# Kernel optimization log

Hardware: AMD Instinct MI355X
Metric: run time of the kernel (lower is better)

## Reference

```python
import jax, jax.numpy as jnp
import numpy as np

D_MODEL = 768
N_HEADS = 12
D_K = 768
D_V = 768
SEQ = 2048
BATCH = 2


def setup_inputs() -> dict:
    key = jax.random.key(0)
    ks = jax.random.split(key, 9)
    s = 0.02
    return {
        "x": jax.random.normal(ks[0], (SEQ, BATCH, D_MODEL), dtype=jnp.float32),
        "Wq": jax.random.normal(ks[1], (D_MODEL, D_K), dtype=jnp.float32) * s,
        "bq": jnp.zeros((D_K,), dtype=jnp.float32),
        "Wk": jax.random.normal(ks[2], (D_MODEL, D_K), dtype=jnp.float32) * s,
        "bk": jnp.zeros((D_K,), dtype=jnp.float32),
        "Wv": jax.random.normal(ks[3], (D_MODEL, D_V), dtype=jnp.float32) * s,
        "bv": jnp.zeros((D_V,), dtype=jnp.float32),
        "Wo": jax.random.normal(ks[4], (D_V, D_MODEL), dtype=jnp.float32) * s,
        "bo": jnp.zeros((D_MODEL,), dtype=jnp.float32),
    }


def reference(x, Wq, bq, Wk, bk, Wv, bv, Wo, bo):
    # x: (S, B, D)
    S, B, D = x.shape
    H = N_HEADS
    hk = D_K // H
    hv = D_V // H
    q = (x @ Wq + bq).reshape(S, B, H, hk)
    k = (x @ Wk + bk).reshape(S, B, H, hk)
    v = (x @ Wv + bv).reshape(S, B, H, hv)
    scale = 1.0 / np.sqrt(hk).astype(np.float32)
    # scores: (B, H, S_q, S_k)
    att = jnp.einsum("sbhd,tbhd->bhst", q, k) * scale
    causal = jnp.triu(jnp.ones((S, S), dtype=bool), k=1)  # True above diagonal
    att = jnp.where(causal, jnp.float32(-jnp.inf), att)
    att = jax.nn.softmax(att, axis=-1)
    y = jnp.einsum("bhst,tbhd->sbhd", att, v).reshape(S, B, D_V)
    return y @ Wo + bo  # (S, B, D)
```

## Files before the change

### kernel.cpp

```cpp
#include <hip/hip_runtime.h>

typedef __attribute__((ext_vector_type(8))) short short8;
typedef __attribute__((ext_vector_type(4))) float f32x4;

#define NHEADS 12
#define SEQLEN 2048
#define HEADD  64
#define DMODEL 768

__device__ __forceinline__ short cvtbf(float f) {
  unsigned u = __builtin_bit_cast(unsigned, f);
  u += 0x7fffu + ((u >> 16) & 1u);
  return (short)(u >> 16);
}

__device__ __forceinline__ void gload16(const void* g, void* l) {
  __builtin_amdgcn_global_load_lds((const __attribute__((address_space(1))) void*)g,
                                   (__attribute__((address_space(3))) void*)l, 16, 0, 0);
}

__device__ __forceinline__ void ds_write_hi16(short* p, float v) {
  asm volatile("ds_write_b16_d16_hi %0, %1"
               : : "v"((__attribute__((address_space(3))) short*)p), "v"(v) : "memory");
}

__global__ void cvt_x_kernel(const float* __restrict__ x, short* __restrict__ o) {
  int i = blockIdx.x * 256 + threadIdx.x;
  const float* p = x + (size_t)i * 8;
  short8 v;
#pragma unroll
  for (int j = 0; j < 8; ++j) v[j] = cvtbf(p[j]);
  *(short8*)(o + (size_t)i * 8) = v;
}

__global__ void transpose_w_kernel(const float* __restrict__ w0, const float* __restrict__ w1,
                                   const float* __restrict__ w2, const float* __restrict__ w3,
                                   short* __restrict__ wt, short* __restrict__ wot) {
  __shared__ float t[32][33];
  const float* W = blockIdx.z == 0 ? w0 : blockIdx.z == 1 ? w1 : blockIdx.z == 2 ? w2 : w3;
  short* O = blockIdx.z < 3 ? wt + (size_t)blockIdx.z * (768 * 768) : wot;
  int tx = threadIdx.x, ty = threadIdx.y;
  int n0 = blockIdx.x * 32, k0 = blockIdx.y * 32;
#pragma unroll
  for (int j = 0; j < 4; ++j)
    t[ty + j * 8][tx] = W[(k0 + ty + j * 8) * 768 + n0 + tx];
  __syncthreads();
#pragma unroll
  for (int j = 0; j < 4; ++j)
    O[(n0 + ty + j * 8) * 768 + k0 + tx] = cvtbf(t[tx][ty + j * 8]);
}

template <int BN>
__device__ __forceinline__ void gemm_core64(const short* __restrict__ A,
                                            const short* __restrict__ Bt,
                                            short* sA, short* sB,
                                            int bm, int bn, f32x4 acc[2][BN / 32]) {
  constexpr int NT = BN / 32;
  const int tid = threadIdx.x;
  const int w = tid >> 6, lane = tid & 63;
  const int quad = lane >> 4, l16 = lane & 15;
  const int wm = (w & 1) * 32, wn = (w >> 1) * (BN / 2);

  int gA[2], lA[2], gB[NT], lB[NT];
#pragma unroll
  for (int j = 0; j < 2; ++j) {
    int slot = j * 256 + w * 64 + lane;
    int r = slot >> 3, c = (slot & 7) ^ (r & 7);
    gA[j] = (bm * 64 + r) * 768 + c * 8;
    lA[j] = (j * 256 + w * 64) * 8;
  }
#pragma unroll
  for (int j = 0; j < NT; ++j) {
    int slot = j * 256 + w * 64 + lane;
    int r = slot >> 3, c = (slot & 7) ^ (r & 7);
    gB[j] = (bn * BN + r) * 768 + c * 8;
    lB[j] = (j * 256 + w * 64) * 8;
  }

  for (int kt = 0; kt < 12; ++kt) {
    __syncthreads();
#pragma unroll
    for (int j = 0; j < 2; ++j) gload16(A + gA[j] + kt * 64, sA + lA[j]);
#pragma unroll
    for (int j = 0; j < NT; ++j) gload16(Bt + gB[j] + kt * 64, sB + lB[j]);
    __syncthreads();
#pragma unroll
    for (int ks = 0; ks < 2; ++ks) {
      short8 a[2], b[NT];
      int cp = (ks * 4 + quad) ^ (l16 & 7);
#pragma unroll
      for (int mt = 0; mt < 2; ++mt)
        a[mt] = *(const short8*)(sA + (wm + mt * 16 + l16) * 64 + cp * 8);
#pragma unroll
      for (int nt = 0; nt < NT; ++nt)
        b[nt] = *(const short8*)(sB + (wn + nt * 16 + l16) * 64 + cp * 8);
#pragma unroll
      for (int mt = 0; mt < 2; ++mt)
#pragma unroll
        for (int nt = 0; nt < NT; ++nt)
          acc[mt][nt] = __builtin_amdgcn_mfma_f32_16x16x32_bf16(a[mt], b[nt], acc[mt][nt], 0, 0, 0);
    }
  }
}

__global__ __launch_bounds__(256, 4) void qkv_gemm(
    const short* __restrict__ A, const short* __restrict__ Bt,
    const float* __restrict__ bq, const float* __restrict__ bk, const float* __restrict__ bv,
    short* __restrict__ oq, short* __restrict__ ok, short* __restrict__ ov) {
  __shared__ short sA[64 * 64];
  __shared__ short sB[128 * 64];
  f32x4 acc[2][4];
  const f32x4 z4 = {0.f, 0.f, 0.f, 0.f};
#pragma unroll
  for (int mt = 0; mt < 2; ++mt)
#pragma unroll
    for (int nt = 0; nt < 4; ++nt) acc[mt][nt] = z4;

  const int bm = blockIdx.x, bn = blockIdx.y;
  gemm_core64<128>(A, Bt, sA, sB, bm, bn, acc);

  const int seg = bn / 6, bn_l = bn % 6;
  const float* bias = seg == 0 ? bq : seg == 1 ? bk : bv;
  short* outp = seg == 0 ? oq : seg == 1 ? ok : ov;

  const int tid = threadIdx.x;
  const int w = tid >> 6, lane = tid & 63;
  const int quad = lane >> 4, l16 = lane & 15;
  const int wm = (w & 1) * 32, wn = (w >> 1) * 64;

#pragma unroll
  for (int nt = 0; nt < 4; ++nt) {
    int n = bn_l * 128 + wn + nt * 16 + l16;
    float bval = bias[n];
    int h = n >> 6, d = n & 63;
#pragma unroll
    for (int mt = 0; mt < 2; ++mt) {
      int rowb = wm + mt * 16 + quad * 4;
#pragma unroll
      for (int r = 0; r < 4; ++r) {
        int m = bm * 64 + rowb + r;
        int s = m >> 1, b = m & 1;
        float v = acc[mt][nt][r] + bval;
        if (seg == 0) v *= 0.1803368801f;
        if (seg < 2)
          outp[((b * NHEADS + h) * SEQLEN + s) * HEADD + d] = cvtbf(v);
        else
          outp[((b * NHEADS + h) * HEADD + d) * SEQLEN + s] = cvtbf(v);
      }
    }
  }
}

#define AE(qi, ts, nt) ((qi) | ((ts) << 8) | ((nt) << 16))
__device__ const int ATTN_TAB[80] = {
  AE(31,0,8), AE(31,8,8), AE(31,16,8), AE(31,24,8),
  AE(30,0,8), AE(30,8,8), AE(30,16,8),
  AE(29,0,8), AE(29,8,8), AE(29,16,8),
  AE(28,0,8), AE(28,8,8), AE(28,16,8),
  AE(27,0,8), AE(27,8,8), AE(27,16,8),
  AE(26,0,8), AE(26,8,8), AE(26,16,8),
  AE(25,0,8), AE(25,8,8), AE(25,16,8),
  AE(24,0,8), AE(24,8,8), AE(24,16,8),
  AE(23,0,8), AE(23,8,8), AE(23,16,8),
  AE(22,0,8), AE(22,8,8),
  AE(21,0,8), AE(21,8,8),
  AE(20,0,8), AE(20,8,8),
  AE(19,0,8), AE(19,8,8),
  AE(18,0,8), AE(18,8,8),
  AE(17,0,8), AE(17,8,8),
  AE(16,0,8), AE(16,8,8),
  AE(15,0,8), AE(15,8,8),
  AE(14,0,8), AE(13,0,8), AE(12,0,8), AE(11,0,8),
  AE(10,0,8), AE(9,0,8),  AE(8,0,8),  AE(7,0,8),
  AE(30,24,7), AE(22,16,7), AE(14,8,7), AE(6,0,7),
  AE(29,24,6), AE(21,16,6), AE(13,8,6), AE(5,0,6),
  AE(28,24,5), AE(20,16,5), AE(12,8,5), AE(4,0,5),
  AE(27,24,4), AE(19,16,4), AE(11,8,4), AE(3,0,4),
  AE(26,24,3), AE(18,16,3), AE(10,8,3), AE(2,0,3),
  AE(25,24,2), AE(17,16,2), AE(9,8,2),  AE(1,0,2),
  AE(24,24,1), AE(16,16,1), AE(8,8,1),  AE(0,0,1),
};
__device__ const int PBASE[32] = {
  0,0,0,0,0,0,0,0,
  0,2,4,6,8,10,12,14,
  16,19,22,25,28,31,34,37,
  40,44,48,52,56,60,64,68};

__global__ __launch_bounds__(256, 4) void attn_kernel(
    const short* __restrict__ Q, const short* __restrict__ K,
    const short* __restrict__ Vt, short* __restrict__ Y,
    float* __restrict__ Of, float* __restrict__ lf) {
  __shared__ short sK[2][64 * 64];
  __shared__ short sV[2][64 * 64];
  __shared__ short sP[64 * 64];
  const int tid = threadIdx.x;
  const int w = tid >> 6, lane = tid & 63;
  const int quad = lane >> 4, l16 = lane & 15;
  const int e = ATTN_TAB[blockIdx.x / 24];
  const int bh = blockIdx.x % 24;
  const int qi = e & 255, ts = (e >> 8) & 255, ntl = e >> 16;
  const int q0 = qi << 6;
  const short* Qb = Q + (size_t)bh * (SEQLEN * HEADD);
  const short* Kb = K + (size_t)bh * (SEQLEN * HEADD);
  const short* Vb = Vt + (size_t)bh * (SEQLEN * HEADD);

  short8 aq[2];
#pragma unroll
  for (int ks = 0; ks < 2; ++ks)
    aq[ks] = *(const short8*)(Qb + (q0 + w * 16 + l16) * 64 + ks * 32 + quad * 8);

  const short8 bones = {0x3F80, 0x3F80, 0x3F80, 0x3F80, 0x3F80, 0x3F80, 0x3F80, 0x3F80};
  f32x4 acc_o[4], acc_l;
  const f32x4 z4 = {0.f, 0.f, 0.f, 0.f};
#pragma unroll
  for (int nt = 0; nt < 4; ++nt) acc_o[nt] = z4;
  acc_l = z4;

  int gK[2], gV[2], lbase[2];
#pragma unroll
  for (int j = 0; j < 2; ++j) {
    int slot = j * 256 + w * 64 + lane;
    int r = slot >> 3, c = (slot & 7) ^ (r & 7);
    gK[j] = r * 64 + c * 8;
    gV[j] = r * 2048 + c * 8;
    lbase[j] = (j * 256 + w * 64) * 8;
  }

  const int qrow = q0 + w * 16 + quad * 4;
  const int tend = ts + ntl;

#pragma unroll
  for (int j = 0; j < 2; ++j) {
    gload16(Kb + (ts << 6) * 64 + gK[j], &sK[0][lbase[j]]);
    gload16(Vb + (ts << 6) + gV[j], &sV[0][lbase[j]]);
  }

  int pb = 0;
  for (int it = ts; it < tend; ++it) {
    __syncthreads();
    if (it + 1 < tend) {
      const int t1 = (it + 1) << 6;
#pragma unroll
      for (int j = 0; j < 2; ++j) {
        gload16(Kb + t1 * 64 + gK[j], &sK[pb ^ 1][lbase[j]]);
        gload16(Vb + t1 + gV[j], &sV[pb ^ 1][lbase[j]]);
      }
    }
    const short* sk = sK[pb];
    const short* sv = sV[pb];

    f32x4 sc[4];
#pragma unroll
    for (int nt = 0; nt < 4; ++nt) sc[nt] = z4;
#pragma unroll
    for (int ks = 0; ks < 2; ++ks) {
      int cp = (ks * 4 + quad) ^ (l16 & 7);
#pragma unroll
      for (int nt = 0; nt < 4; ++nt) {
        short8 bk = *(const short8*)(sk + (nt * 16 + l16) * 64 + cp * 8);
        sc[nt] = __builtin_amdgcn_mfma_f32_16x16x32_bf16(aq[ks], bk, sc[nt], 0, 0, 0);
      }
    }

    if (it == qi) {
      const int t0 = it << 6;
#pragma unroll
      for (int nt = 0; nt < 4; ++nt)
#pragma unroll
        for (int r = 0; r < 4; ++r) {
          int t = t0 + nt * 16 + l16;
          if (t > qrow + r) sc[nt][r] = -1e30f;
        }
    }

#pragma unroll
    for (int nt = 0; nt < 4; ++nt)
#pragma unroll
      for (int r = 0; r < 4; ++r) {
        float p = __builtin_amdgcn_exp2f(sc[nt][r]);
        int rq = w * 16 + quad * 4 + r;
        int t = nt * 16 + l16;
        int c = t >> 3;
        ds_write_hi16(&sP[rq * 64 + ((c ^ (rq & 7)) * 8 + (t & 7))], p);
      }

#pragma unroll
    for (int kst = 0; kst < 2; ++kst) {
      int rq = w * 16 + l16;
      int cpa = (kst * 4 + quad) ^ (rq & 7);
      short8 ap = *(const short8*)(sP + rq * 64 + cpa * 8);
      acc_l = __builtin_amdgcn_mfma_f32_16x16x32_bf16(ap, bones, acc_l, 0, 0, 0);
#pragma unroll
      for (int nt = 0; nt < 4; ++nt) {
        int row = nt * 16 + l16;
        int cv = (kst * 4 + quad) ^ (row & 7);
        short8 bv = *(const short8*)(sv + row * 64 + cv * 8);
        acc_o[nt] = __builtin_amdgcn_mfma_f32_16x16x32_bf16(ap, bv, acc_o[nt], 0, 0, 0);
      }
    }
    pb ^= 1;
  }

  if (qi < 8) {
    const int b = bh / NHEADS, h = bh % NHEADS;
#pragma unroll
    for (int r = 0; r < 4; ++r) {
      float rl = __builtin_amdgcn_rcpf(acc_l[r]);
      int srow = q0 + w * 16 + quad * 4 + r;
#pragma unroll
      for (int nt = 0; nt < 4; ++nt)
        Y[(srow * 2 + b) * DMODEL + h * 64 + nt * 16 + l16] = cvtbf(acc_o[nt][r] * rl);
    }
  } else {
    const int slot = bh * 72 + PBASE[qi] + (ts >> 3);
    float* Ob = Of + (size_t)slot * 4096;
#pragma unroll
    for (int r = 0; r < 4; ++r) {
      int row = w * 16 + quad * 4 + r;
#pragma unroll
      for (int nt = 0; nt < 4; ++nt)
        Ob[row * 64 + nt * 16 + l16] = acc_o[nt][r];
      if (l16 == 0) lf[slot * 64 + row] = acc_l[r];
    }
  }
}

__global__ void attn_merge(const float* __restrict__ Of, const float* __restrict__ lf,
                           short* __restrict__ Y) {
  const int bh = blockIdx.x % 24, qi = 8 + blockIdx.x / 24;
  const int nch = (qi >> 3) + 1;
  const int base = bh * 72 + PBASE[qi];
  const float* O0 = Of + (size_t)base * 4096;
  const float* L0 = lf + base * 64;
  const int b = bh / NHEADS, h = bh % NHEADS;
  const int tid = threadIdx.x;
#pragma unroll
  for (int j = 0; j < 16; ++j) {
    int idx = j * 256 + tid;
    int row = idx >> 6, col = idx & 63;
    float o = 0.f, l = 0.f;
    for (int c = 0; c < nch; ++c) {
      o += O0[c * 4096 + idx];
      l += L0[c * 64 + row];
    }
    float v = o * __builtin_amdgcn_rcpf(l);
    int srow = qi * 64 + row;
    Y[(srow * 2 + b) * DMODEL + h * 64 + col] = cvtbf(v);
  }
}

__global__ __launch_bounds__(256, 4) void oproj_gemm(
    const short* __restrict__ A, const short* __restrict__ Bt,
    const float* __restrict__ bo, float* __restrict__ out) {
  __shared__ short sA[64 * 64];
  __shared__ short sB[64 * 64];
  f32x4 acc[2][2];
  const f32x4 z4 = {0.f, 0.f, 0.f, 0.f};
#pragma unroll
  for (int mt = 0; mt < 2; ++mt)
#pragma unroll
    for (int nt = 0; nt < 2; ++nt) acc[mt][nt] = z4;

  const int bm = blockIdx.x, bn = blockIdx.y;
  gemm_core64<64>(A, Bt, sA, sB, bm, bn, acc);

  const int tid = threadIdx.x;
  const int w = tid >> 6, lane = tid & 63;
  const int quad = lane >> 4, l16 = lane & 15;
  const int wm = (w & 1) * 32, wn = (w >> 1) * 32;

#pragma unroll
  for (int nt = 0; nt < 2; ++nt) {
    int n = bn * 64 + wn + nt * 16 + l16;
    float bval = bo[n];
#pragma unroll
    for (int mt = 0; mt < 2; ++mt) {
      int rowb = wm + mt * 16 + quad * 4;
#pragma unroll
      for (int r = 0; r < 4; ++r) {
        int m = bm * 64 + rowb + r;
        out[(size_t)m * 768 + n] = acc[mt][nt][r] + bval;
      }
    }
  }
}

extern "C" void kernel_launch(void* const* d_in, const int* in_sizes, int n_in,
                              void* d_out, int out_size, void* d_ws, size_t ws_size,
                              hipStream_t stream) {
  const float* x  = (const float*)d_in[0];
  const float* Wq = (const float*)d_in[1];
  const float* bq = (const float*)d_in[2];
  const float* Wk = (const float*)d_in[3];
  const float* bk = (const float*)d_in[4];
  const float* Wv = (const float*)d_in[5];
  const float* bv = (const float*)d_in[6];
  const float* Wo = (const float*)d_in[7];
  const float* bo = (const float*)d_in[8];
  float* out = (float*)d_out;

  short* ws  = (short*)d_ws;
  short* xb  = ws;
  short* wt  = ws + 3145728;
  short* wot = ws + 4915200;
  short* qw  = ws + 5505024;
  short* kw  = ws + 8650752;
  short* vw  = ws + 11796480;
  short* yw  = ws + 14942208;
  float* Of  = (float*)(ws + 18087936);
  float* lf  = Of + 7077888;

  cvt_x_kernel<<<1536, 256, 0, stream>>>(x, xb);
  transpose_w_kernel<<<dim3(24, 24, 4), dim3(32, 8), 0, stream>>>(Wq, Wk, Wv, Wo, wt, wot);
  qkv_gemm<<<dim3(64, 18), 256, 0, stream>>>(xb, wt, bq, bk, bv, qw, kw, vw);
  attn_kernel<<<1920, 256, 0, stream>>>(qw, kw, vw, yw, Of, lf);
  attn_merge<<<576, 256, 0, stream>>>(Of, lf, yw);
  oproj_gemm<<<dim3(64, 12), 256, 0, stream>>>(yw, wot, bo, out);
}
```

Baseline: 168.1 us.

## Fuse prep kernels, enlarge GEMM tiles to 128x128, double-buffer oproj, vectorize merge

Merges the x conversion and weight transpose into one launch so there is one fewer kernel dispatch. Both GEMMs move from 64-row tiles to 128x128 tiles, which gives more MFMA work per LDS load. The output projection also gets a double-buffered LDS pipeline so the next tile's global loads overlap the current tile's compute. attn_merge now reads and writes 4-wide vectors. The larger tiles shrink the grids (576 and 192 blocks) and raise register and LDS use, which can hurt occupancy and leave CUs underfilled, especially for oproj with only 192 blocks.

```diff
diff --git a/kernel.cpp b/kernel.cpp
--- a/kernel.cpp
+++ b/kernel.cpp
@@ -1,6 +1,7 @@
 #include <hip/hip_runtime.h>
 
 typedef __attribute__((ext_vector_type(8))) short short8;
+typedef __attribute__((ext_vector_type(4))) short s16x4;
 typedef __attribute__((ext_vector_type(4))) float f32x4;
 
 #define NHEADS 12
@@ -24,23 +25,28 @@
                : : "v"((__attribute__((address_space(3))) short*)p), "v"(v) : "memory");
 }
 
-__global__ void cvt_x_kernel(const float* __restrict__ x, short* __restrict__ o) {
-  int i = blockIdx.x * 256 + threadIdx.x;
-  const float* p = x + (size_t)i * 8;
-  short8 v;
-#pragma unroll
-  for (int j = 0; j < 8; ++j) v[j] = cvtbf(p[j]);
-  *(short8*)(o + (size_t)i * 8) = v;
-}
-
-__global__ void transpose_w_kernel(const float* __restrict__ w0, const float* __restrict__ w1,
-                                   const float* __restrict__ w2, const float* __restrict__ w3,
-                                   short* __restrict__ wt, short* __restrict__ wot) {
+__global__ void prep_kernel(const float* __restrict__ x, short* __restrict__ xb,
+                            const float* __restrict__ w0, const float* __restrict__ w1,
+                            const float* __restrict__ w2, const float* __restrict__ w3,
+                            short* __restrict__ wt, short* __restrict__ wot) {
   __shared__ float t[32][33];
-  const float* W = blockIdx.z == 0 ? w0 : blockIdx.z == 1 ? w1 : blockIdx.z == 2 ? w2 : w3;
-  short* O = blockIdx.z < 3 ? wt + (size_t)blockIdx.z * (768 * 768) : wot;
-  int tx = threadIdx.x, ty = threadIdx.y;
-  int n0 = blockIdx.x * 32, k0 = blockIdx.y * 32;
+  const int tid = threadIdx.x;
+  if (blockIdx.x < 1536) {
+    int i = blockIdx.x * 256 + tid;
+    const float* p = x + (size_t)i * 8;
+    short8 v;
+#pragma unroll
+    for (int j = 0; j < 8; ++j) v[j] = cvtbf(p[j]);
+    *(short8*)(xb + (size_t)i * 8) = v;
+    return;
+  }
+  int bx = blockIdx.x - 1536;
+  int bz = bx / 576, rem = bx - bz * 576;
+  int bxx = rem % 24, byy = rem / 24;
+  const float* W = bz == 0 ? w0 : bz == 1 ? w1 : bz == 2 ? w2 : w3;
+  short* O = bz < 3 ? wt + (size_t)bz * (768 * 768) : wot;
+  int tx = tid & 31, ty = tid >> 5;
+  int n0 = bxx * 32, k0 = byy * 32;
 #pragma unroll
   for (int j = 0; j < 4; ++j)
     t[ty + j * 8][tx] = W[(k0 + ty + j * 8) * 768 + n0 + tx];
@@ -50,74 +56,107 @@
     O[(n0 + ty + j * 8) * 768 + k0 + tx] = cvtbf(t[tx][ty + j * 8]);
 }
 
-template <int BN>
-__device__ __forceinline__ void gemm_core64(const short* __restrict__ A,
-                                            const short* __restrict__ Bt,
-                                            short* sA, short* sB,
-                                            int bm, int bn, f32x4 acc[2][BN / 32]) {
-  constexpr int NT = BN / 32;
+template <bool DBUF>
+__device__ __forceinline__ void gemm_core128(const short* __restrict__ A,
+                                             const short* __restrict__ Bt,
+                                             short* sA, short* sB,
+                                             int bm, int bn, f32x4 acc[4][4]) {
   const int tid = threadIdx.x;
   const int w = tid >> 6, lane = tid & 63;
   const int quad = lane >> 4, l16 = lane & 15;
-  const int wm = (w & 1) * 32, wn = (w >> 1) * (BN / 2);
-
-  int gA[2], lA[2], gB[NT], lB[NT];
-#pragma unroll
-  for (int j = 0; j < 2; ++j) {
+  const int wm = (w & 1) * 64, wn = (w >> 1) * 64;
+
+  int gA[4], gB[4], lbase[4];
+#pragma unroll
+  for (int j = 0; j < 4; ++j) {
     int slot = j * 256 + w * 64 + lane;
     int r = slot >> 3, c = (slot & 7) ^ (r & 7);
-    gA[j] = (bm * 64 + r) * 768 + c * 8;
-    lA[j] = (j * 256 + w * 64) * 8;
-  }
-#pragma unroll
-  for (int j = 0; j < NT; ++j) {
-    int slot = j * 256 + w * 64 + lane;
-    int r = slot >> 3, c = (slot & 7) ^ (r & 7);
-    gB[j] = (bn * BN + r) * 768 + c * 8;
-    lB[j] = (j * 256 + w * 64) * 8;
-  }
-
-  for (int kt = 0; kt < 12; ++kt) {
-    __syncthreads();
-#pragma unroll
-    for (int j = 0; j < 2; ++j) gload16(A + gA[j] + kt * 64, sA + lA[j]);
-#pragma unroll
-    for (int j = 0; j < NT; ++j) gload16(Bt + gB[j] + kt * 64, sB + lB[j]);
-    __syncthreads();
-#pragma unroll
-    for (int ks = 0; ks < 2; ++ks) {
-      short8 a[2], b[NT];
-      int cp = (ks * 4 + quad) ^ (l16 & 7);
-#pragma unroll
-      for (int mt = 0; mt < 2; ++mt)
-        a[mt] = *(const short8*)(sA + (wm + mt * 16 + l16) * 64 + cp * 8);
-#pragma unroll
-      for (int nt = 0; nt < NT; ++nt)
-        b[nt] = *(const short8*)(sB + (wn + nt * 16 + l16) * 64 + cp * 8);
-#pragma unroll
-      for (int mt = 0; mt < 2; ++mt)
-#pragma unroll
-        for (int nt = 0; nt < NT; ++nt)
-          acc[mt][nt] = __builtin_amdgcn_mfma_f32_16x16x32_bf16(a[mt], b[nt], acc[mt][nt], 0, 0, 0);
-    }
-  }
-}
-
-__global__ __launch_bounds__(256, 4) void qkv_gemm(
+    gA[j] = (bm * 128 + r) * 768 + c * 8;
+    gB[j] = (bn * 128 + r) * 768 + c * 8;
+    lbase[j] = (j * 256 + w * 64) * 8;
+  }
+
+  if (DBUF) {
+#pragma unroll
+    for (int j = 0; j < 4; ++j) {
+      gload16(A + gA[j], sA + lbase[j]);
+      gload16(Bt + gB[j], sB + lbase[j]);
+    }
+    int pb = 0;
+    for (int kt = 0; kt < 12; ++kt) {
+      __syncthreads();
+      if (kt + 1 < 12) {
+        int o = (pb ^ 1) * 8192;
+#pragma unroll
+        for (int j = 0; j < 4; ++j) {
+          gload16(A + gA[j] + (kt + 1) * 64, sA + o + lbase[j]);
+          gload16(Bt + gB[j] + (kt + 1) * 64, sB + o + lbase[j]);
+        }
+      }
+      const short* pa = sA + pb * 8192;
+      const short* pbv = sB + pb * 8192;
+#pragma unroll
+      for (int ks = 0; ks < 2; ++ks) {
+        int cp = (ks * 4 + quad) ^ (l16 & 7);
+        short8 a[4], b[4];
+#pragma unroll
+        for (int mt = 0; mt < 4; ++mt)
+          a[mt] = *(const short8*)(pa + (wm + mt * 16 + l16) * 64 + cp * 8);
+#pragma unroll
+        for (int nt = 0; nt < 4; ++nt)
+          b[nt] = *(const short8*)(pbv + (wn + nt * 16 + l16) * 64 + cp * 8);
+#pragma unroll
+        for (int mt = 0; mt < 4; ++mt)
+#pragma unroll
+          for (int nt = 0; nt < 4; ++nt)
+            acc[mt][nt] = __builtin_amdgcn_mfma_f32_16x16x32_bf16(a[mt], b[nt], acc[mt][nt], 0, 0, 0);
+      }
+      pb ^= 1;
+    }
+  } else {
+    for (int kt = 0; kt < 12; ++kt) {
+      __syncthreads();
+#pragma unroll
+      for (int j = 0; j < 4; ++j) {
+        gload16(A + gA[j] + kt * 64, sA + lbase[j]);
+        gload16(Bt + gB[j] + kt * 64, sB + lbase[j]);
+      }
+      __syncthreads();
+#pragma unroll
+      for (int ks = 0; ks < 2; ++ks) {
+        int cp = (ks * 4 + quad) ^ (l16 & 7);
+        short8 a[4], b[4];
+#pragma unroll
+        for (int mt = 0; mt < 4; ++mt)
+          a[mt] = *(const short8*)(sA + (wm + mt * 16 + l16) * 64 + cp * 8);
+#pragma unroll
+        for (int nt = 0; nt < 4; ++nt)
+          b[nt] = *(const short8*)(sB + (wn + nt * 16 + l16) * 64 + cp * 8);
+#pragma unroll
+        for (int mt = 0; mt < 4; ++mt)
+#pragma unroll
+          for (int nt = 0; nt < 4; ++nt)
+            acc[mt][nt] = __builtin_amdgcn_mfma_f32_16x16x32_bf16(a[mt], b[nt], acc[mt][nt], 0, 0, 0);
+      }
+    }
+  }
+}
+
+__global__ __launch_bounds__(256, 3) void qkv_gemm(
     const short* __restrict__ A, const short* __restrict__ Bt,
     const float* __restrict__ bq, const float* __restrict__ bk, const float* __restrict__ bv,
     short* __restrict__ oq, short* __restrict__ ok, short* __restrict__ ov) {
-  __shared__ short sA[64 * 64];
+  __shared__ short sA[128 * 64];
   __shared__ short sB[128 * 64];
-  f32x4 acc[2][4];
+  f32x4 acc[4][4];
   const f32x4 z4 = {0.f, 0.f, 0.f, 0.f};
 #pragma unroll
-  for (int mt = 0; mt < 2; ++mt)
+  for (int mt = 0; mt < 4; ++mt)
 #pragma unroll
     for (int nt = 0; nt < 4; ++nt) acc[mt][nt] = z4;
 
   const int bm = blockIdx.x, bn = blockIdx.y;
-  gemm_core64<128>(A, Bt, sA, sB, bm, bn, acc);
+  gemm_core128<false>(A, Bt, sA, sB, bm, bn, acc);
 
   const int seg = bn / 6, bn_l = bn % 6;
   const float* bias = seg == 0 ? bq : seg == 1 ? bk : bv;
@@ -126,7 +165,7 @@
   const int tid = threadIdx.x;
   const int w = tid >> 6, lane = tid & 63;
   const int quad = lane >> 4, l16 = lane & 15;
-  const int wm = (w & 1) * 32, wn = (w >> 1) * 64;
+  const int wm = (w & 1) * 64, wn = (w >> 1) * 64;
 
 #pragma unroll
   for (int nt = 0; nt < 4; ++nt) {
@@ -134,11 +173,11 @@
     float bval = bias[n];
     int h = n >> 6, d = n & 63;
 #pragma unroll
-    for (int mt = 0; mt < 2; ++mt) {
+    for (int mt = 0; mt < 4; ++mt) {
       int rowb = wm + mt * 16 + quad * 4;
 #pragma unroll
       for (int r = 0; r < 4; ++r) {
-        int m = bm * 64 + rowb + r;
+        int m = bm * 128 + rowb + r;
         int s = m >> 1, b = m & 1;
         float v = acc[mt][nt][r] + bval;
         if (seg == 0) v *= 0.1803368801f;
@@ -335,50 +374,54 @@
   const int b = bh / NHEADS, h = bh % NHEADS;
   const int tid = threadIdx.x;
 #pragma unroll
-  for (int j = 0; j < 16; ++j) {
-    int idx = j * 256 + tid;
-    int row = idx >> 6, col = idx & 63;
-    float o = 0.f, l = 0.f;
-    for (int c = 0; c < nch; ++c) {
-      o += O0[c * 4096 + idx];
+  for (int j = 0; j < 4; ++j) {
+    int i4 = j * 256 + tid;
+    int row = i4 >> 4, col4 = (i4 & 15) * 4;
+    f32x4 o = *(const f32x4*)(O0 + (size_t)i4 * 4);
+    float l = L0[row];
+    for (int c = 1; c < nch; ++c) {
+      o += *(const f32x4*)(O0 + (size_t)c * 4096 + (size_t)i4 * 4);
       l += L0[c * 64 + row];
     }
-    float v = o * __builtin_amdgcn_rcpf(l);
+    float rl = __builtin_amdgcn_rcpf(l);
+    s16x4 y;
+#pragma unroll
+    for (int k = 0; k < 4; ++k) y[k] = cvtbf(o[k] * rl);
     int srow = qi * 64 + row;
-    Y[(srow * 2 + b) * DMODEL + h * 64 + col] = cvtbf(v);
-  }
-}
-
-__global__ __launch_bounds__(256, 4) void oproj_gemm(
+    *(s16x4*)(Y + (size_t)(srow * 2 + b) * DMODEL + h * 64 + col4) = y;
+  }
+}
+
+__global__ __launch_bounds__(256, 2) void oproj_gemm(
     const short* __restrict__ A, const short* __restrict__ Bt,
     const float* __restrict__ bo, float* __restrict__ out) {
-  __shared__ short sA[64 * 64];
-  __shared__ short sB[64 * 64];
-  f32x4 acc[2][2];
+  __shared__ short sA[2 * 128 * 64];
+  __shared__ short sB[2 * 128 * 64];
+  f32x4 acc[4][4];
   const f32x4 z4 = {0.f, 0.f, 0.f, 0.f};
 #pragma unroll
-  for (int mt = 0; mt < 2; ++mt)
-#pragma unroll
-    for (int nt = 0; nt < 2; ++nt) acc[mt][nt] = z4;
+  for (int mt = 0; mt < 4; ++mt)
+#pragma unroll
+    for (int nt = 0; nt < 4; ++nt) acc[mt][nt] = z4;
 
   const int bm = blockIdx.x, bn = blockIdx.y;
-  gemm_core64<64>(A, Bt, sA, sB, bm, bn, acc);
+  gemm_core128<true>(A, Bt, sA, sB, bm, bn, acc);
 
   const int tid = threadIdx.x;
   const int w = tid >> 6, lane = tid & 63;
   const int quad = lane >> 4, l16 = lane & 15;
-  const int wm = (w & 1) * 32, wn = (w >> 1) * 32;
-
-#pragma unroll
-  for (int nt = 0; nt < 2; ++nt) {
-    int n = bn * 64 + wn + nt * 16 + l16;
+  const int wm = (w & 1) * 64, wn = (w >> 1) * 64;
+
+#pragma unroll
+  for (int nt = 0; nt < 4; ++nt) {
+    int n = bn * 128 + wn + nt * 16 + l16;
     float bval = bo[n];
 #pragma unroll
-    for (int mt = 0; mt < 2; ++mt) {
+    for (int mt = 0; mt < 4; ++mt) {
       int rowb = wm + mt * 16 + quad * 4;
 #pragma unroll
       for (int r = 0; r < 4; ++r) {
-        int m = bm * 64 + rowb + r;
+        int m = bm * 128 + rowb + r;
         out[(size_t)m * 768 + n] = acc[mt][nt][r] + bval;
       }
     }
@@ -410,10 +453,9 @@
   float* Of  = (float*)(ws + 18087936);
   float* lf  = Of + 7077888;
 
-  cvt_x_kernel<<<1536, 256, 0, stream>>>(x, xb);
-  transpose_w_kernel<<<dim3(24, 24, 4), dim3(32, 8), 0, stream>>>(Wq, Wk, Wv, Wo, wt, wot);
-  qkv_gemm<<<dim3(64, 18), 256, 0, stream>>>(xb, wt, bq, bk, bv, qw, kw, vw);
+  prep_kernel<<<3840, 256, 0, stream>>>(x, xb, Wq, Wk, Wv, Wo, wt, wot);
+  qkv_gemm<<<dim3(32, 18), 256, 0, stream>>>(xb, wt, bq, bk, bv, qw, kw, vw);
   attn_kernel<<<1920, 256, 0, stream>>>(qw, kw, vw, yw, Of, lf);
   attn_merge<<<576, 256, 0, stream>>>(Of, lf, yw);
-  oproj_gemm<<<dim3(64, 12), 256, 0, stream>>>(yw, wot, bo, out);
-}
+  oproj_gemm<<<dim3(32, 6), 256, 0, stream>>>(yw, wot, bo, out);
+}
```

New measurement: 153.4 us. 1.1x faster.
